# Performance work log

Hardware: AMD Instinct MI355X
Metric: run time of the kernel (lower is better)

Reference implementation:

```python
import jax, jax.numpy as jnp
import numpy as np

B, L, C, H, RATIO = 2, 512, 256, 8, 4
D = C // H
EPS = 1e-5


def layernorm(x, g, b):
    m = jnp.mean(x, axis=-1, keepdims=True)
    v = jnp.mean((x - m) ** 2, axis=-1, keepdims=True)
    return (x - m) * jax.lax.rsqrt(v + EPS) * g + b


def setup_inputs() -> dict:
    key = jax.random.key(0)
    ks = jax.random.split(key, 10)
    s = 0.02
    return {
        "x": jax.random.normal(ks[0], (B, L, C), jnp.float32),
        "relative_pos": jax.random.normal(ks[1], (B, L, L, C), jnp.float32),
        # attention params (qkv_bias=False)
        "w_qkv": jax.random.normal(ks[2], (C, 3 * C), jnp.float32) * s,
        "w_proj": jax.random.normal(ks[3], (C, C), jnp.float32) * s,
        "b_proj": jnp.zeros((C,), jnp.float32),
        # relative_project: Linear(C,H) -> GELU -> LayerNorm(H)
        "w_rel": jax.random.normal(ks[4], (C, H), jnp.float32) * s,
        "b_rel": jnp.zeros((H,), jnp.float32),
        "g_reln": jnp.ones((H,), jnp.float32),
        "b_reln": jnp.zeros((H,), jnp.float32),
        # block layernorms
        "g_n1": jnp.ones((C,), jnp.float32),
        "b_n1": jnp.zeros((C,), jnp.float32),
        "g_n2": jnp.ones((C,), jnp.float32),
        "b_n2": jnp.zeros((C,), jnp.float32),
        # MLP (mlp_ratio=4, act=GELU)
        "w_mlp1": jax.random.normal(ks[5], (C, RATIO * C), jnp.float32) * s,
        "b_mlp1": jnp.zeros((RATIO * C,), jnp.float32),
        "w_mlp2": jax.random.normal(ks[6], (RATIO * C, C), jnp.float32) * s,
        "b_mlp2": jnp.zeros((C,), jnp.float32),
    }


def reference(x, relative_pos, w_qkv, w_proj, b_proj, w_rel, b_rel,
              g_reln, b_reln, g_n1, b_n1, g_n2, b_n2,
              w_mlp1, b_mlp1, w_mlp2, b_mlp2):
    # eval mode: dropout / droppath are identity
    scale = D ** -0.5

    # --- attention branch ---
    h = layernorm(x, g_n1, b_n1)                      # [B,L,C]
    qkv = (h @ w_qkv).reshape(B, L, 3, H, D)
    qkv = jnp.transpose(qkv, (2, 0, 3, 1, 4))          # [3,B,H,L,D]
    q, k, v = qkv[0], qkv[1], qkv[2]

    attn = jnp.einsum("bhid,bhjd->bhij", q, k)        # [B,H,L,L]

    # relative bias: Linear -> GELU(exact) -> LayerNorm over heads
    rel = jax.nn.gelu(relative_pos @ w_rel + b_rel, approximate=False)  # [B,L,L,H]
    rel = layernorm(rel, g_reln, b_reln)
    rel = jnp.transpose(rel, (0, 3, 1, 2))            # [B,H,L,L]

    attn = jax.nn.softmax((attn + rel) * scale, axis=-1)
    o = jnp.einsum("bhij,bhjd->bhid", attn, v)        # [B,H,L,D]
    o = jnp.transpose(o, (0, 2, 1, 3)).reshape(B, L, C)
    o = o @ w_proj + b_proj
    x = x + o

    # --- MLP branch (jump=False since out_feat==in_feat) ---
    h = layernorm(x, g_n2, b_n2)
    h = jax.nn.gelu(h @ w_mlp1 + b_mlp1, approximate=False)
    h = h @ w_mlp2 + b_mlp2
    return x + h
```

## Files before the change

kernel.cpp:

```cpp
#include <hip/hip_runtime.h>
#include <hip/hip_bf16.h>
#include <cstddef>

#define EPS_ 1e-5f
#define SCALE_ 0.1767766952966369f

typedef short bf16x8_t __attribute__((ext_vector_type(8)));
typedef float f32x4_t  __attribute__((ext_vector_type(4)));

__device__ __forceinline__ float gelu_f(float x) {
    float y = 0.7978845608028654f * (x + 0.044715f * x * x * x);
    float e = __expf(2.0f * y);
    float t = 1.0f - 2.0f * __builtin_amdgcn_rcpf(e + 1.0f);
    return 0.5f * x * (1.0f + t);
}
__device__ __forceinline__ unsigned short f2bf(float f) {
    return __builtin_bit_cast(unsigned short, __float2bfloat16(f));
}
__device__ __forceinline__ unsigned f2bf2(float a, float b) {
    unsigned lo = __builtin_bit_cast(unsigned short, __float2bfloat16(a));
    unsigned hi = __builtin_bit_cast(unsigned short, __float2bfloat16(b));
    return lo | (hi << 16);
}

__device__ __forceinline__ void ln_row_body(const float* __restrict__ x,
                                            const float* __restrict__ g,
                                            const float* __restrict__ b,
                                            unsigned short* __restrict__ out,
                                            int row, int lane) {
    const float4 xv = *(const float4*)(x + (size_t)row * 256 + lane * 4);
    float s  = xv.x + xv.y + xv.z + xv.w;
    float sq = xv.x*xv.x + xv.y*xv.y + xv.z*xv.z + xv.w*xv.w;
#pragma unroll
    for (int m = 1; m < 64; m <<= 1) { s += __shfl_xor(s, m); sq += __shfl_xor(sq, m); }
    float mean = s * (1.0f/256.0f);
    float var  = sq * (1.0f/256.0f) - mean*mean;
    float rstd = rsqrtf(var + EPS_);
    float4 gv = *(const float4*)(g + lane*4);
    float4 bv = *(const float4*)(b + lane*4);
    uint2 o;
    o.x = f2bf2((xv.x-mean)*rstd*gv.x + bv.x, (xv.y-mean)*rstd*gv.y + bv.y);
    o.y = f2bf2((xv.z-mean)*rstd*gv.z + bv.z, (xv.w-mean)*rstd*gv.w + bv.w);
    *(uint2*)(out + (size_t)row * 256 + lane * 4) = o;
}

__global__ __launch_bounds__(256) void prep_kernel(
    const float* __restrict__ w_qkv,  unsigned short* __restrict__ wqkvT,
    const float* __restrict__ w_mlp1, unsigned short* __restrict__ wmlp1T,
    const float* __restrict__ w_mlp2, unsigned short* __restrict__ wmlp2T,
    const float* __restrict__ x, const float* __restrict__ g_n1,
    const float* __restrict__ b_n1, unsigned short* __restrict__ hbf) {
    __shared__ float tile[32][33];
    int bid = blockIdx.x, t = threadIdx.x;
    if (bid >= 704) {
        ln_row_body(x, g_n1, b_n1, hbf, (bid - 704) * 4 + (t >> 6), t & 63);
        return;
    }
    const float* W; unsigned short* WT; int K, N, tt;
    if (bid < 192)      { W = w_qkv;  WT = wqkvT;  K = 256;  N = 768;  tt = bid; }
    else if (bid < 448) { W = w_mlp1; WT = wmlp1T; K = 256;  N = 1024; tt = bid - 192; }
    else                { W = w_mlp2; WT = wmlp2T; K = 1024; N = 256;  tt = bid - 448; }
    int ntn = N >> 5;
    int kt = tt / ntn, nt = tt % ntn;
    int k0 = kt * 32, n0 = nt * 32;
    {
        int kr = t >> 3, cg = (t & 7) * 4;
        float4 v = *(const float4*)(W + (size_t)(k0 + kr) * N + n0 + cg);
        tile[kr][cg+0] = v.x; tile[kr][cg+1] = v.y; tile[kr][cg+2] = v.z; tile[kr][cg+3] = v.w;
    }
    __syncthreads();
    {
        int nr = t >> 3, kg = (t & 7) * 4;
        uint2 o;
        o.x = f2bf2(tile[kg+0][nr], tile[kg+1][nr]);
        o.y = f2bf2(tile[kg+2][nr], tile[kg+3][nr]);
        *(uint2*)(WT + (size_t)(n0 + nr) * K + k0 + kg) = o;
    }
}

template<bool BIAS, bool GACT, bool BF16OUT, int KSPLIT>
__global__ __launch_bounds__(256) void mgemm_kernel(
    const unsigned short* __restrict__ A, const unsigned short* __restrict__ BT,
    const float* __restrict__ bias,
    void* __restrict__ Cout, int M, int N, int K) {
    __shared__ unsigned short Al[64][40];
    __shared__ unsigned short Bl[64][40];
    int t = threadIdx.x;
    int bm = blockIdx.x, bn = blockIdx.y, kz = blockIdx.z;
    int kchunk = K / KSPLIT;
    int srow = t >> 2, skk = (t & 3) * 8;
    const unsigned short* Ap = A  + (size_t)(bm*64 + srow) * K + kz*kchunk + skk;
    const unsigned short* Bp = BT + (size_t)(bn*64 + srow) * K + kz*kchunk + skk;
    int lane = t & 63, w = t >> 6, wr = w >> 1, wc = w & 1;
    int fr = lane & 15, fg = lane >> 4;
    f32x4_t a00 = {0.f,0.f,0.f,0.f}, a01 = {0.f,0.f,0.f,0.f};
    f32x4_t a10 = {0.f,0.f,0.f,0.f}, a11 = {0.f,0.f,0.f,0.f};
    for (int kk = 0; kk < kchunk; kk += 32) {
        uint4 av = *(const uint4*)(Ap + kk);
        uint4 bv = *(const uint4*)(Bp + kk);
        __syncthreads();
        *(uint4*)&Al[srow][skk] = av;
        *(uint4*)&Bl[srow][skk] = bv;
        __syncthreads();
        bf16x8_t fa0 = *(const bf16x8_t*)&Al[wr*32      + fr][fg*8];
        bf16x8_t fa1 = *(const bf16x8_t*)&Al[wr*32 + 16 + fr][fg*8];
        bf16x8_t fb0 = *(const bf16x8_t*)&Bl[wc*32      + fr][fg*8];
        bf16x8_t fb1 = *(const bf16x8_t*)&Bl[wc*32 + 16 + fr][fg*8];
        a00 = __builtin_amdgcn_mfma_f32_16x16x32_bf16(fa0, fb0, a00, 0, 0, 0);
        a01 = __builtin_amdgcn_mfma_f32_16x16x32_bf16(fa0, fb1, a01, 0, 0, 0);
        a10 = __builtin_amdgcn_mfma_f32_16x16x32_bf16(fa1, fb0, a10, 0, 0, 0);
        a11 = __builtin_amdgcn_mfma_f32_16x16x32_bf16(fa1, fb1, a11, 0, 0, 0);
    }
    float* Cf = (float*)Cout + (KSPLIT > 1 ? (size_t)kz * M * N : (size_t)0);
    unsigned short* Cb = (unsigned short*)Cout;
    auto emit = [&](f32x4_t acc, int mi, int ni) {
        int Ro = bm*64 + wr*32 + mi*16 + fg*4;
        int Co = bn*64 + wc*32 + ni*16 + fr;
        float bval = BIAS ? bias[Co] : 0.f;
#pragma unroll
        for (int e = 0; e < 4; ++e) {
            int r = Ro + e;
            float v = acc[e];
            if (BIAS)  v += bval;
            if (GACT)  v = gelu_f(v);
            if (BF16OUT) Cb[(size_t)r * N + Co] = f2bf(v);
            else         Cf[(size_t)r * N + Co] = v;
        }
    };
    emit(a00, 0, 0); emit(a01, 0, 1); emit(a10, 1, 0); emit(a11, 1, 1);
}

__global__ __launch_bounds__(256) void qk_kernel(const float* __restrict__ qkv,
                                                 float* __restrict__ qk) {
    __shared__ float k_lds[512*32];
    int t = threadIdx.x;
    int it = blockIdx.x;
    int h  = blockIdx.y;
    int b  = blockIdx.z;
    const float* base = qkv + (size_t)b * 393216;
#pragma unroll
    for (int r = 0; r < 16; ++r) {
        int idx = r*256 + t;
        int row = idx >> 3, c4 = idx & 7;
        float4 kv = *(const float4*)(base + (size_t)row*768 + 256 + h*32 + c4*4);
        *(float4*)(k_lds + row*32 + c4*4) = kv;
    }
    __syncthreads();
    int ir = t & 31, jg = t >> 5;
    int i = it*32 + ir;
    float4 q[8];
    const float* qp = base + (size_t)i*768 + h*32;
#pragma unroll
    for (int c4 = 0; c4 < 8; ++c4) q[c4] = *(const float4*)(qp + c4*4);
    float* outp = qk + (((size_t)(b*512 + i))*8 + h)*512 + jg*64;
    for (int jj = 0; jj < 64; jj += 4) {
        float a4[4];
#pragma unroll
        for (int u = 0; u < 4; ++u) {
            const float* kp = k_lds + (size_t)(jg*64 + jj + u)*32;
            float acc = 0.f;
#pragma unroll
            for (int c4 = 0; c4 < 8; ++c4) {
                float4 kv = *(const float4*)(kp + c4*4);
                acc += q[c4].x*kv.x + q[c4].y*kv.y + q[c4].z*kv.z + q[c4].w*kv.w;
            }
            a4[u] = acc;
        }
        *(float4*)(outp + jj) = make_float4(a4[0], a4[1], a4[2], a4[3]);
    }
}

#define LGS 520
__global__ __launch_bounds__(256) void rel_mega_kernel(
    const float* __restrict__ rp, const float* __restrict__ qk,
    const float* __restrict__ qkv,
    const float* __restrict__ w_rel, const float* __restrict__ b_rel,
    const float* __restrict__ g_reln, const float* __restrict__ b_reln,
    const float* __restrict__ w_proj, const float* __restrict__ b_proj,
    const float* __restrict__ x, const float* __restrict__ g_n2,
    const float* __restrict__ b_n2,
    float* __restrict__ x1_out, unsigned short* __restrict__ h2bf) {
    __shared__ float lg_lds[8*LGS];
    __shared__ float o_lds[256];
    __shared__ float red[8];
    int t = threadIdx.x;
    int bi = blockIdx.x;
    int b  = bi >> 9;
    int wid = t >> 6, lane = t & 63;
    int fr = lane & 15, fg = lane >> 4;
    bool act = fr < 8;
    bf16x8_t bfrag[8];
#pragma unroll
    for (int kk = 0; kk < 8; ++kk) {
        bf16x8_t bf;
#pragma unroll
        for (int e = 0; e < 8; ++e) {
            float v = act ? w_rel[(size_t)(kk*32 + fg*8 + e)*8 + fr] : 0.f;
            bf[e] = (short)f2bf(v);
        }
        bfrag[kk] = bf;
    }
    const float* rpb = rp + (size_t)bi * 512 * 256;
#pragma unroll 1
    for (int tile = 0; tile < 8; ++tile) {
        int j0 = wid*128 + tile*16;
        const float* arow = rpb + (size_t)(j0 + fr)*256 + fg*8;
        f32x4_t acc = {0.f,0.f,0.f,0.f};
#pragma unroll
        for (int kk = 0; kk < 8; ++kk) {
            float4 x0 = *(const float4*)(arow + kk*32);
            float4 x1 = *(const float4*)(arow + kk*32 + 4);
            union { bf16x8_t v; uint4 u; } cvt;
            cvt.u.x = f2bf2(x0.x, x0.y);
            cvt.u.y = f2bf2(x0.z, x0.w);
            cvt.u.z = f2bf2(x1.x, x1.y);
            cvt.u.w = f2bf2(x1.z, x1.w);
            acc = __builtin_amdgcn_mfma_f32_16x16x32_bf16(cvt.v, bfrag[kk], acc, 0, 0, 0);
        }
        if (act) {
#pragma unroll
            for (int r = 0; r < 4; ++r)
                lg_lds[fr*LGS + j0 + fg*4 + r] = acc[r];
        }
    }
    __syncthreads();
#pragma unroll
    for (int rep = 0; rep < 2; ++rep) {
        int j = t + rep*256;
        float gv[8];
        float sm = 0.f, sq = 0.f;
#pragma unroll
        for (int h = 0; h < 8; ++h) {
            float val = lg_lds[h*LGS + j] + b_rel[h];
            float g = gelu_f(val);
            gv[h] = g; sm += g; sq += g*g;
        }
        float mean = sm * 0.125f;
        float var  = sq * 0.125f - mean*mean;
        float rstd = rsqrtf(var + EPS_);
#pragma unroll
        for (int h = 0; h < 8; ++h)
            lg_lds[h*LGS + j] = (gv[h] - mean) * rstd * g_reln[h] + b_reln[h];
    }
    __syncthreads();
    {
        int h = wid*2 + (lane >> 5);
        int sub = lane & 31;
        float* row = lg_lds + h*LGS;
        const float* qrow = qk + ((size_t)bi*8 + h)*512;
        float v[16];
#pragma unroll
        for (int c4 = 0; c4 < 4; ++c4) {
            float4 r4 = *(const float4*)(row  + c4*128 + sub*4);
            float4 q4 = *(const float4*)(qrow + c4*128 + sub*4);
            v[c4*4+0] = (q4.x + r4.x) * SCALE_;
            v[c4*4+1] = (q4.y + r4.y) * SCALE_;
            v[c4*4+2] = (q4.z + r4.z) * SCALE_;
            v[c4*4+3] = (q4.w + r4.w) * SCALE_;
        }
        float mx = v[0];
#pragma unroll
        for (int e = 1; e < 16; ++e) mx = fmaxf(mx, v[e]);
#pragma unroll
        for (int m = 1; m < 32; m <<= 1) mx = fmaxf(mx, __shfl_xor(mx, m));
        float s = 0.f;
#pragma unroll
        for (int e = 0; e < 16; ++e) { v[e] = __expf(v[e] - mx); s += v[e]; }
#pragma unroll
        for (int m = 1; m < 32; m <<= 1) s += __shfl_xor(s, m);
        float inv = 1.0f / s;
#pragma unroll
        for (int e = 0; e < 16; ++e) v[e] *= inv;
#pragma unroll
        for (int c4 = 0; c4 < 4; ++c4) {
            float4 o4 = make_float4(v[c4*4+0], v[c4*4+1], v[c4*4+2], v[c4*4+3]);
            *(float4*)(row + c4*128 + sub*4) = o4;
        }
    }
    __syncthreads();
    {
        int c = t, h = c >> 5;
        const float* vcol = qkv + (size_t)b*393216 + 512 + c;
        const float* arow = lg_lds + h*LGS;
        float acc = 0.f;
        for (int j = 0; j < 512; j += 4) {
            float4 a4 = *(const float4*)(arow + j);
            acc += a4.x * vcol[(size_t)(j+0)*768];
            acc += a4.y * vcol[(size_t)(j+1)*768];
            acc += a4.z * vcol[(size_t)(j+2)*768];
            acc += a4.w * vcol[(size_t)(j+3)*768];
        }
        o_lds[c] = acc;
    }
    __syncthreads();
    float x1c;
    {
        int c = t;
        float acc2 = 0.f;
        for (int k = 0; k < 256; k += 4) {
            acc2 += o_lds[k+0] * w_proj[(size_t)(k+0)*256 + c];
            acc2 += o_lds[k+1] * w_proj[(size_t)(k+1)*256 + c];
            acc2 += o_lds[k+2] * w_proj[(size_t)(k+2)*256 + c];
            acc2 += o_lds[k+3] * w_proj[(size_t)(k+3)*256 + c];
        }
        x1c = x[(size_t)bi*256 + c] + b_proj[c] + acc2;
        x1_out[(size_t)bi*256 + c] = x1c;
    }
    {
        float s = x1c, sq = x1c*x1c;
#pragma unroll
        for (int m = 1; m < 64; m <<= 1) { s += __shfl_xor(s, m); sq += __shfl_xor(sq, m); }
        if (lane == 0) { red[wid*2] = s; red[wid*2+1] = sq; }
        __syncthreads();
        float S  = red[0] + red[2] + red[4] + red[6];
        float SQ = red[1] + red[3] + red[5] + red[7];
        float mean = S * (1.0f/256.0f);
        float var  = SQ * (1.0f/256.0f) - mean*mean;
        float rstd = rsqrtf(var + EPS_);
        float h2 = (x1c - mean) * rstd * g_n2[t] + b_n2[t];
        h2bf[(size_t)bi*256 + t] = f2bf(h2);
    }
}

__global__ __launch_bounds__(256) void combine_kernel(const float* __restrict__ part,
                                                      const float* __restrict__ bias,
                                                      const float* __restrict__ resid,
                                                      float* __restrict__ out) {
    int f = blockIdx.x * 256 + threadIdx.x;
    int e = f * 4;
    float4 r  = *(const float4*)(resid + e);
    float4 bv = *(const float4*)(bias + (e & 255));
    float4 p0 = *(const float4*)(part + e);
    float4 p1 = *(const float4*)(part + 262144 + e);
    float4 p2 = *(const float4*)(part + 524288 + e);
    float4 p3 = *(const float4*)(part + 786432 + e);
    float4 o4;
    o4.x = r.x + bv.x + p0.x + p1.x + p2.x + p3.x;
    o4.y = r.y + bv.y + p0.y + p1.y + p2.y + p3.y;
    o4.z = r.z + bv.z + p0.z + p1.z + p2.z + p3.z;
    o4.w = r.w + bv.w + p0.w + p1.w + p2.w + p3.w;
    *(float4*)(out + e) = o4;
}

extern "C" void kernel_launch(void* const* d_in, const int* in_sizes, int n_in,
                              void* d_out, int out_size, void* d_ws, size_t ws_size,
                              hipStream_t stream) {
    const float* x      = (const float*)d_in[0];
    const float* rp     = (const float*)d_in[1];
    const float* w_qkv  = (const float*)d_in[2];
    const float* w_proj = (const float*)d_in[3];
    const float* b_proj = (const float*)d_in[4];
    const float* w_rel  = (const float*)d_in[5];
    const float* b_rel  = (const float*)d_in[6];
    const float* g_reln = (const float*)d_in[7];
    const float* b_reln = (const float*)d_in[8];
    const float* g_n1   = (const float*)d_in[9];
    const float* b_n1   = (const float*)d_in[10];
    const float* g_n2   = (const float*)d_in[11];
    const float* b_n2   = (const float*)d_in[12];
    const float* w_mlp1 = (const float*)d_in[13];
    const float* b_mlp1 = (const float*)d_in[14];
    const float* w_mlp2 = (const float*)d_in[15];
    const float* b_mlp2 = (const float*)d_in[16];
    float* out = (float*)d_out;

    float* ws      = (float*)d_ws;
    float* ws_qkv  = ws;
    float* ws_qk   = ws_qkv + 786432;
    float* ws_x1   = ws_qk  + 4194304;
    float* ws_pt   = ws_x1  + 262144;
    unsigned short* ub = (unsigned short*)(ws_pt + 1048576);
    unsigned short* hbf    = ub;
    unsigned short* h2bf   = hbf  + 262144;
    unsigned short* hgbf   = h2bf + 262144;
    unsigned short* wqkvT  = hgbf + 1048576;
    unsigned short* wmlp1T = wqkvT + 196608;
    unsigned short* wmlp2T = wmlp1T + 262144;

    prep_kernel<<<960, 256, 0, stream>>>(w_qkv, wqkvT, w_mlp1, wmlp1T, w_mlp2, wmlp2T,
                                         x, g_n1, b_n1, hbf);
    mgemm_kernel<false,false,false,1><<<dim3(16,12,1), 256, 0, stream>>>(
        hbf, wqkvT, nullptr, ws_qkv, 1024, 768, 256);
    qk_kernel<<<dim3(16,8,2), 256, 0, stream>>>(ws_qkv, ws_qk);
    rel_mega_kernel<<<1024, 256, 0, stream>>>(rp, ws_qk, ws_qkv, w_rel, b_rel,
                                              g_reln, b_reln, w_proj, b_proj,
                                              x, g_n2, b_n2, ws_x1, h2bf);
    mgemm_kernel<true,true,true,1><<<dim3(16,16,1), 256, 0, stream>>>(
        h2bf, wmlp1T, b_mlp1, hgbf, 1024, 1024, 256);
    mgemm_kernel<false,false,false,4><<<dim3(16,4,4), 256, 0, stream>>>(
        hgbf, wmlp2T, nullptr, ws_pt, 1024, 256, 1024);
    combine_kernel<<<256, 256, 0, stream>>>(ws_pt, b_mlp2, ws_x1, out);
}
```

Measured before the change: 198.3 us.

## Process two query rows per rel block and atomically accumulate split-K MLP2 into output

The relative-bias mega kernel now handles two query rows per block, so V-column and w_proj loads are shared across both rows and the grid is halved. It writes x1 plus the MLP2 bias directly into the output. The final split-K GEMM then atomically adds its partial sums into that output, which removes the partial-sum buffer and the separate combine kernel. In exchange, float atomics make the summation order nondeterministic, and halving the grid to 512 blocks with doubled LDS per block may lower occupancy on the bandwidth-heavy relative_pos read.

Result: no change. 201.0 us (+1.4%).

```diff
diff --git a/kernel.cpp b/kernel.cpp
--- a/kernel.cpp
+++ b/kernel.cpp
@@ -78,7 +78,7 @@
     }
 }
 
-template<bool BIAS, bool GACT, bool BF16OUT, int KSPLIT>
+template<bool BIAS, bool GACT, bool BF16OUT, int KSPLIT, bool ATOMIC>
 __global__ __launch_bounds__(256) void mgemm_kernel(
     const unsigned short* __restrict__ A, const unsigned short* __restrict__ BT,
     const float* __restrict__ bias,
@@ -111,7 +111,7 @@
         a10 = __builtin_amdgcn_mfma_f32_16x16x32_bf16(fa1, fb0, a10, 0, 0, 0);
         a11 = __builtin_amdgcn_mfma_f32_16x16x32_bf16(fa1, fb1, a11, 0, 0, 0);
     }
-    float* Cf = (float*)Cout + (KSPLIT > 1 ? (size_t)kz * M * N : (size_t)0);
+    float* Cf = (float*)Cout;
     unsigned short* Cb = (unsigned short*)Cout;
     auto emit = [&](f32x4_t acc, int mi, int ni) {
         int Ro = bm*64 + wr*32 + mi*16 + fg*4;
@@ -123,8 +123,9 @@
             float v = acc[e];
             if (BIAS)  v += bval;
             if (GACT)  v = gelu_f(v);
-            if (BF16OUT) Cb[(size_t)r * N + Co] = f2bf(v);
-            else         Cf[(size_t)r * N + Co] = v;
+            if (ATOMIC)      atomicAdd(&Cf[(size_t)r * N + Co], v);
+            else if (BF16OUT) Cb[(size_t)r * N + Co] = f2bf(v);
+            else              Cf[(size_t)r * N + Co] = v;
         }
     };
     emit(a00, 0, 0); emit(a01, 0, 1); emit(a10, 1, 0); emit(a11, 1, 1);
@@ -178,14 +179,14 @@
     const float* __restrict__ g_reln, const float* __restrict__ b_reln,
     const float* __restrict__ w_proj, const float* __restrict__ b_proj,
     const float* __restrict__ x, const float* __restrict__ g_n2,
-    const float* __restrict__ b_n2,
-    float* __restrict__ x1_out, unsigned short* __restrict__ h2bf) {
-    __shared__ float lg_lds[8*LGS];
-    __shared__ float o_lds[256];
+    const float* __restrict__ b_n2, const float* __restrict__ b_mlp2,
+    float* __restrict__ out, unsigned short* __restrict__ h2bf) {
+    __shared__ float lg_lds[2][8*LGS];
+    __shared__ float o_lds[2][256];
     __shared__ float red[8];
     int t = threadIdx.x;
-    int bi = blockIdx.x;
-    int b  = bi >> 9;
+    int bi0 = blockIdx.x * 2;
+    int b  = bi0 >> 9;
     int wid = t >> 6, lane = t & 63;
     int fr = lane & 15, fg = lane >> 4;
     bool act = fr < 8;
@@ -200,54 +201,66 @@
         }
         bfrag[kk] = bf;
     }
-    const float* rpb = rp + (size_t)bi * 512 * 256;
+    const float* rpb0 = rp + (size_t)bi0 * 512 * 256;
+    const float* rpb1 = rpb0 + 512 * 256;
 #pragma unroll 1
     for (int tile = 0; tile < 8; ++tile) {
         int j0 = wid*128 + tile*16;
-        const float* arow = rpb + (size_t)(j0 + fr)*256 + fg*8;
-        f32x4_t acc = {0.f,0.f,0.f,0.f};
+        const float* arow0 = rpb0 + (size_t)(j0 + fr)*256 + fg*8;
+        const float* arow1 = rpb1 + (size_t)(j0 + fr)*256 + fg*8;
+        f32x4_t acc0 = {0.f,0.f,0.f,0.f};
+        f32x4_t acc1 = {0.f,0.f,0.f,0.f};
 #pragma unroll
         for (int kk = 0; kk < 8; ++kk) {
-            float4 x0 = *(const float4*)(arow + kk*32);
-            float4 x1 = *(const float4*)(arow + kk*32 + 4);
-            union { bf16x8_t v; uint4 u; } cvt;
-            cvt.u.x = f2bf2(x0.x, x0.y);
-            cvt.u.y = f2bf2(x0.z, x0.w);
-            cvt.u.z = f2bf2(x1.x, x1.y);
-            cvt.u.w = f2bf2(x1.z, x1.w);
-            acc = __builtin_amdgcn_mfma_f32_16x16x32_bf16(cvt.v, bfrag[kk], acc, 0, 0, 0);
+            float4 p0 = *(const float4*)(arow0 + kk*32);
+            float4 p1 = *(const float4*)(arow0 + kk*32 + 4);
+            float4 q0 = *(const float4*)(arow1 + kk*32);
+            float4 q1 = *(const float4*)(arow1 + kk*32 + 4);
+            union { bf16x8_t v; uint4 u; } c0, c1;
+            c0.u.x = f2bf2(p0.x, p0.y); c0.u.y = f2bf2(p0.z, p0.w);
+            c0.u.z = f2bf2(p1.x, p1.y); c0.u.w = f2bf2(p1.z, p1.w);
+            c1.u.x = f2bf2(q0.x, q0.y); c1.u.y = f2bf2(q0.z, q0.w);
+            c1.u.z = f2bf2(q1.x, q1.y); c1.u.w = f2bf2(q1.z, q1.w);
+            acc0 = __builtin_amdgcn_mfma_f32_16x16x32_bf16(c0.v, bfrag[kk], acc0, 0, 0, 0);
+            acc1 = __builtin_amdgcn_mfma_f32_16x16x32_bf16(c1.v, bfrag[kk], acc1, 0, 0, 0);
         }
         if (act) {
 #pragma unroll
-            for (int r = 0; r < 4; ++r)
-                lg_lds[fr*LGS + j0 + fg*4 + r] = acc[r];
-        }
-    }
-    __syncthreads();
-#pragma unroll
-    for (int rep = 0; rep < 2; ++rep) {
-        int j = t + rep*256;
-        float gv[8];
-        float sm = 0.f, sq = 0.f;
-#pragma unroll
-        for (int h = 0; h < 8; ++h) {
-            float val = lg_lds[h*LGS + j] + b_rel[h];
-            float g = gelu_f(val);
-            gv[h] = g; sm += g; sq += g*g;
-        }
-        float mean = sm * 0.125f;
-        float var  = sq * 0.125f - mean*mean;
-        float rstd = rsqrtf(var + EPS_);
-#pragma unroll
-        for (int h = 0; h < 8; ++h)
-            lg_lds[h*LGS + j] = (gv[h] - mean) * rstd * g_reln[h] + b_reln[h];
-    }
-    __syncthreads();
-    {
+            for (int r = 0; r < 4; ++r) {
+                lg_lds[0][fr*LGS + j0 + fg*4 + r] = acc0[r];
+                lg_lds[1][fr*LGS + j0 + fg*4 + r] = acc1[r];
+            }
+        }
+    }
+    __syncthreads();
+#pragma unroll
+    for (int rr = 0; rr < 2; ++rr) {
+#pragma unroll
+        for (int rep = 0; rep < 2; ++rep) {
+            int j = t + rep*256;
+            float gv[8];
+            float sm = 0.f, sq = 0.f;
+#pragma unroll
+            for (int h = 0; h < 8; ++h) {
+                float val = lg_lds[rr][h*LGS + j] + b_rel[h];
+                float g = gelu_f(val);
+                gv[h] = g; sm += g; sq += g*g;
+            }
+            float mean = sm * 0.125f;
+            float var  = sq * 0.125f - mean*mean;
+            float rstd = rsqrtf(var + EPS_);
+#pragma unroll
+            for (int h = 0; h < 8; ++h)
+                lg_lds[rr][h*LGS + j] = (gv[h] - mean) * rstd * g_reln[h] + b_reln[h];
+        }
+    }
+    __syncthreads();
+#pragma unroll
+    for (int rr = 0; rr < 2; ++rr) {
         int h = wid*2 + (lane >> 5);
         int sub = lane & 31;
-        float* row = lg_lds + h*LGS;
-        const float* qrow = qk + ((size_t)bi*8 + h)*512;
+        float* row = lg_lds[rr] + h*LGS;
+        const float* qrow = qk + ((size_t)(bi0+rr)*8 + h)*512;
         float v[16];
 #pragma unroll
         for (int c4 = 0; c4 < 4; ++c4) {
@@ -281,35 +294,48 @@
     {
         int c = t, h = c >> 5;
         const float* vcol = qkv + (size_t)b*393216 + 512 + c;
-        const float* arow = lg_lds + h*LGS;
-        float acc = 0.f;
+        const float* a0 = lg_lds[0] + h*LGS;
+        const float* a1 = lg_lds[1] + h*LGS;
+        float acc0 = 0.f, acc1 = 0.f;
         for (int j = 0; j < 512; j += 4) {
-            float4 a4 = *(const float4*)(arow + j);
-            acc += a4.x * vcol[(size_t)(j+0)*768];
-            acc += a4.y * vcol[(size_t)(j+1)*768];
-            acc += a4.z * vcol[(size_t)(j+2)*768];
-            acc += a4.w * vcol[(size_t)(j+3)*768];
-        }
-        o_lds[c] = acc;
-    }
-    __syncthreads();
-    float x1c;
+            float vv0 = vcol[(size_t)(j+0)*768];
+            float vv1 = vcol[(size_t)(j+1)*768];
+            float vv2 = vcol[(size_t)(j+2)*768];
+            float vv3 = vcol[(size_t)(j+3)*768];
+            float4 p0 = *(const float4*)(a0 + j);
+            float4 p1 = *(const float4*)(a1 + j);
+            acc0 += p0.x*vv0 + p0.y*vv1 + p0.z*vv2 + p0.w*vv3;
+            acc1 += p1.x*vv0 + p1.y*vv1 + p1.z*vv2 + p1.w*vv3;
+        }
+        o_lds[0][c] = acc0;
+        o_lds[1][c] = acc1;
+    }
+    __syncthreads();
+    float x1a, x1b;
     {
         int c = t;
-        float acc2 = 0.f;
+        float accA = 0.f, accB = 0.f;
         for (int k = 0; k < 256; k += 4) {
-            acc2 += o_lds[k+0] * w_proj[(size_t)(k+0)*256 + c];
-            acc2 += o_lds[k+1] * w_proj[(size_t)(k+1)*256 + c];
-            acc2 += o_lds[k+2] * w_proj[(size_t)(k+2)*256 + c];
-            acc2 += o_lds[k+3] * w_proj[(size_t)(k+3)*256 + c];
-        }
-        x1c = x[(size_t)bi*256 + c] + b_proj[c] + acc2;
-        x1_out[(size_t)bi*256 + c] = x1c;
-    }
-    {
-        float s = x1c, sq = x1c*x1c;
+            float w0 = w_proj[(size_t)(k+0)*256 + c];
+            float w1 = w_proj[(size_t)(k+1)*256 + c];
+            float w2 = w_proj[(size_t)(k+2)*256 + c];
+            float w3 = w_proj[(size_t)(k+3)*256 + c];
+            accA += o_lds[0][k]*w0 + o_lds[0][k+1]*w1 + o_lds[0][k+2]*w2 + o_lds[0][k+3]*w3;
+            accB += o_lds[1][k]*w0 + o_lds[1][k+1]*w1 + o_lds[1][k+2]*w2 + o_lds[1][k+3]*w3;
+        }
+        float bp = b_proj[c], bm = b_mlp2[c];
+        x1a = x[(size_t)bi0*256 + c] + bp + accA;
+        x1b = x[(size_t)(bi0+1)*256 + c] + bp + accB;
+        out[(size_t)bi0*256 + c]     = x1a + bm;
+        out[(size_t)(bi0+1)*256 + c] = x1b + bm;
+    }
+#pragma unroll
+    for (int rr = 0; rr < 2; ++rr) {
+        float xv = (rr == 0) ? x1a : x1b;
+        float s = xv, sq = xv*xv;
 #pragma unroll
         for (int m = 1; m < 64; m <<= 1) { s += __shfl_xor(s, m); sq += __shfl_xor(sq, m); }
+        __syncthreads();
         if (lane == 0) { red[wid*2] = s; red[wid*2+1] = sq; }
         __syncthreads();
         float S  = red[0] + red[2] + red[4] + red[6];
@@ -317,29 +343,9 @@
         float mean = S * (1.0f/256.0f);
         float var  = SQ * (1.0f/256.0f) - mean*mean;
         float rstd = rsqrtf(var + EPS_);
-        float h2 = (x1c - mean) * rstd * g_n2[t] + b_n2[t];
-        h2bf[(size_t)bi*256 + t] = f2bf(h2);
-    }
-}
-
-__global__ __launch_bounds__(256) void combine_kernel(const float* __restrict__ part,
-                                                      const float* __restrict__ bias,
-                                                      const float* __restrict__ resid,
-                                                      float* __restrict__ out) {
-    int f = blockIdx.x * 256 + threadIdx.x;
-    int e = f * 4;
-    float4 r  = *(const float4*)(resid + e);
-    float4 bv = *(const float4*)(bias + (e & 255));
-    float4 p0 = *(const float4*)(part + e);
-    float4 p1 = *(const float4*)(part + 262144 + e);
-    float4 p2 = *(const float4*)(part + 524288 + e);
-    float4 p3 = *(const float4*)(part + 786432 + e);
-    float4 o4;
-    o4.x = r.x + bv.x + p0.x + p1.x + p2.x + p3.x;
-    o4.y = r.y + bv.y + p0.y + p1.y + p2.y + p3.y;
-    o4.z = r.z + bv.z + p0.z + p1.z + p2.z + p3.z;
-    o4.w = r.w + bv.w + p0.w + p1.w + p2.w + p3.w;
-    *(float4*)(out + e) = o4;
+        float h2 = (xv - mean) * rstd * g_n2[t] + b_n2[t];
+        h2bf[(size_t)(bi0+rr)*256 + t] = f2bf(h2);
+    }
 }
 
 extern "C" void kernel_launch(void* const* d_in, const int* in_sizes, int n_in,
@@ -367,9 +373,7 @@
     float* ws      = (float*)d_ws;
     float* ws_qkv  = ws;
     float* ws_qk   = ws_qkv + 786432;
-    float* ws_x1   = ws_qk  + 4194304;
-    float* ws_pt   = ws_x1  + 262144;
-    unsigned short* ub = (unsigned short*)(ws_pt + 1048576);
+    unsigned short* ub = (unsigned short*)(ws_qk + 4194304);
     unsigned short* hbf    = ub;
     unsigned short* h2bf   = hbf  + 262144;
     unsigned short* hgbf   = h2bf + 262144;
@@ -379,15 +383,14 @@
 
     prep_kernel<<<960, 256, 0, stream>>>(w_qkv, wqkvT, w_mlp1, wmlp1T, w_mlp2, wmlp2T,
                                          x, g_n1, b_n1, hbf);
-    mgemm_kernel<false,false,false,1><<<dim3(16,12,1), 256, 0, stream>>>(
+    mgemm_kernel<false,false,false,1,false><<<dim3(16,12,1), 256, 0, stream>>>(
         hbf, wqkvT, nullptr, ws_qkv, 1024, 768, 256);
     qk_kernel<<<dim3(16,8,2), 256, 0, stream>>>(ws_qkv, ws_qk);
-    rel_mega_kernel<<<1024, 256, 0, stream>>>(rp, ws_qk, ws_qkv, w_rel, b_rel,
-                                              g_reln, b_reln, w_proj, b_proj,
-                                              x, g_n2, b_n2, ws_x1, h2bf);
-    mgemm_kernel<true,true,true,1><<<dim3(16,16,1), 256, 0, stream>>>(
+    rel_mega_kernel<<<512, 256, 0, stream>>>(rp, ws_qk, ws_qkv, w_rel, b_rel,
+                                             g_reln, b_reln, w_proj, b_proj,
+                                             x, g_n2, b_n2, b_mlp2, out, h2bf);
+    mgemm_kernel<true,true,true,1,false><<<dim3(16,16,1), 256, 0, stream>>>(
         h2bf, wmlp1T, b_mlp1, hgbf, 1024, 1024, 256);
-    mgemm_kernel<false,false,false,4><<<dim3(16,4,4), 256, 0, stream>>>(
-        hgbf, wmlp2T, nullptr, ws_pt, 1024, 256, 1024);
-    combine_kernel<<<256, 256, 0, stream>>>(ws_pt, b_mlp2, ws_x1, out);
-}
+    mgemm_kernel<false,false,false,4,true><<<dim3(16,4,4), 256, 0, stream>>>(
+        hgbf, wmlp2T, nullptr, out, 1024, 256, 1024);
+}
```
